# Performance work log

Measured on AMD Instinct MI355X. Metric: run time of the kernel, lower is better.

Reference implementation:

```python
import jax, jax.numpy as jnp
import numpy as np

B, T, C, N = 4, 2048, 1024, 16
D = C // N


def setup_inputs() -> dict:
    key = jax.random.key(0)
    ks = jax.random.split(key, 10)
    s = 1.0 / np.sqrt(C)
    x = jax.random.normal(ks[0], (B, T, C), dtype=jnp.float32)
    token_mask = jax.random.randint(ks[1], (B, T), 0, 2, dtype=jnp.int32)
    token_mask = token_mask.at[:, 0].set(1)  # keep col 0 valid so no all--inf row
    inp = {"x": x, "token_mask": token_mask}
    for i, name in enumerate(["q", "k", "v", "p"]):
        inp[f"w{name}"] = jax.random.uniform(ks[2 + 2 * i], (C, C), jnp.float32, -s, s)
        inp[f"b{name}"] = jax.random.uniform(ks[3 + 2 * i], (C,), jnp.float32, -s, s)
    return inp


def reference(x, token_mask, wq, bq, wk, bk, wv, bv, wp, bp):
    # projections: nn.Linear computes x @ W.T + b
    q = (x @ wq.T + bq).reshape(B, T, N, D)
    k = (x @ wk.T + bk).reshape(B, T, N, D)
    v = (x @ wv.T + bv).reshape(B, T, N, D)
    # scores: (B, N, T, T)
    scores = jnp.einsum("bqnd,bknd->bnqk", q, k) / jnp.sqrt(jnp.float32(D))
    causal = jnp.tril(jnp.ones((T, T), dtype=bool))
    valid = causal[None, None] & (token_mask[:, None, None, :] != 0)
    scores = jnp.where(valid, scores, -jnp.inf)
    probs = jax.nn.softmax(scores, axis=-1)
    attn = jnp.einsum("bnqk,bknd->bqnd", probs, v).reshape(B, T, C)
    out = attn @ wp.T + bp
    return out
```

## Files before the change

kernel.cpp:

```cpp
#include <hip/hip_runtime.h>
#include <math.h>

typedef short bf16x8 __attribute__((ext_vector_type(8)));
typedef float f32x4 __attribute__((ext_vector_type(4)));

__device__ __forceinline__ unsigned short f2bf(float f) {
    union { float f; unsigned u; } v; v.f = f;
    unsigned r = v.u + 0x7fffu + ((v.u >> 16) & 1u);
    return (unsigned short)(r >> 16);
}

__device__ __forceinline__ void gld_lds16(const unsigned short* g, const unsigned short* l) {
    __builtin_amdgcn_global_load_lds(
        (const __attribute__((address_space(1))) void*)g,
        (__attribute__((address_space(3))) void*)l, 16, 0, 0);
}

__global__ void cvt_f32_bf16(const float* __restrict__ src, unsigned short* __restrict__ dst, int n) {
    int i = (blockIdx.x * blockDim.x + threadIdx.x) * 4;
    if (i < n) {
        float4 f = *(const float4*)(src + i);
        ushort4 o;
        o.x = f2bf(f.x); o.y = f2bf(f.y); o.z = f2bf(f.z); o.w = f2bf(f.w);
        *(ushort4*)(dst + i) = o;
    }
}

__global__ void cvt4_f32_bf16(const float* s0, const float* s1, const float* s2, const float* s3,
                              unsigned short* d0, unsigned short* d1, unsigned short* d2,
                              unsigned short* d3, int n) {
    const float* s; unsigned short* d;
    switch (blockIdx.y) {
        case 0: s = s0; d = d0; break;
        case 1: s = s1; d = d1; break;
        case 2: s = s2; d = d2; break;
        default: s = s3; d = d3; break;
    }
    int i = (blockIdx.x * blockDim.x + threadIdx.x) * 4;
    if (i < n) {
        float4 f = *(const float4*)(s + i);
        ushort4 o;
        o.x = f2bf(f.x); o.y = f2bf(f.y); o.z = f2bf(f.z); o.w = f2bf(f.w);
        *(ushort4*)(d + i) = o;
    }
}

__global__ __launch_bounds__(256) void gemm_bt(
        const unsigned short* __restrict__ A, const unsigned short* __restrict__ W,
        const float* __restrict__ bias, float* __restrict__ outF,
        unsigned short* __restrict__ outB, int M, int N, int K) {
    __shared__ __align__(16) unsigned short As[128][32];
    __shared__ __align__(16) unsigned short Ws[128][32];
    const int m0 = blockIdx.y * 128, n0 = blockIdx.x * 128;
    const int tid = threadIdx.x, lane = tid & 63, w = tid >> 6;
    const int quad = lane >> 4, lc = lane & 15;
    const int wr = (w >> 1) * 64, wc = (w & 1) * 64;
    const int sr = lane >> 2, sc = (lane & 3) * 8;

    f32x4 acc[4][4] = {};

    for (int k0 = 0; k0 < K; k0 += 32) {
        __syncthreads();
        gld_lds16(A + (size_t)(m0 + w * 32 +      sr) * K + k0 + sc, &As[w * 32     ][0]);
        gld_lds16(A + (size_t)(m0 + w * 32 + 16 + sr) * K + k0 + sc, &As[w * 32 + 16][0]);
        gld_lds16(W + (size_t)(n0 + w * 32 +      sr) * K + k0 + sc, &Ws[w * 32     ][0]);
        gld_lds16(W + (size_t)(n0 + w * 32 + 16 + sr) * K + k0 + sc, &Ws[w * 32 + 16][0]);
        __syncthreads();
        bf16x8 af[4], bw[4];
        #pragma unroll
        for (int i = 0; i < 4; ++i) af[i] = *(const bf16x8*)&As[wr + i * 16 + lc][quad * 8];
        #pragma unroll
        for (int j = 0; j < 4; ++j) bw[j] = *(const bf16x8*)&Ws[wc + j * 16 + lc][quad * 8];
        #pragma unroll
        for (int i = 0; i < 4; ++i)
            #pragma unroll
            for (int j = 0; j < 4; ++j)
                acc[i][j] = __builtin_amdgcn_mfma_f32_16x16x32_bf16(af[i], bw[j], acc[i][j], 0, 0, 0);
    }

    #pragma unroll
    for (int j = 0; j < 4; ++j) {
        int col = n0 + wc + j * 16 + lc;
        float bj = bias[col];
        #pragma unroll
        for (int i = 0; i < 4; ++i) {
            int rowb = m0 + wr + i * 16 + quad * 4;
            #pragma unroll
            for (int r = 0; r < 4; ++r) {
                float v = acc[i][j][r] + bj;
                size_t idx = (size_t)(rowb + r) * N + col;
                if (outB) outB[idx] = f2bf(v);
                else      outF[idx] = v;
            }
        }
    }
}

__global__ __launch_bounds__(256, 4) void attn_kernel(
        const unsigned short* __restrict__ Q, const unsigned short* __restrict__ K,
        const unsigned short* __restrict__ V, const int* __restrict__ tmask,
        unsigned short* __restrict__ O) {
    const int T = 2048, C = 1024;
    __shared__ __align__(16) unsigned short Kl[64][72];
    __shared__ __align__(16) unsigned short VT[64][72];
    __shared__ __align__(16) unsigned short Pl[4][16][72];
    __shared__ float maskf[64];

    const int pair = blockIdx.x;
    const int bn = blockIdx.y;
    const int b = bn >> 4, h = bn & 15;
    const int tid = threadIdx.x, w = tid >> 6, lane = tid & 63;
    const int quad = lane >> 4, lc = lane & 15;
    const float NEG_INF = -__builtin_inff();

    #pragma unroll 1
    for (int half = 0; half < 2; ++half) {
        const int qt = half ? (31 - pair) : pair;

        size_t qrow = (size_t)(b * T + qt * 64 + w * 16 + lc) * C + h * 64;
        bf16x8 qb0 = *(const bf16x8*)(Q + qrow + quad * 8);
        bf16x8 qb1 = *(const bf16x8*)(Q + qrow + 32 + quad * 8);

        f32x4 oaccT[4] = {};
        float m = NEG_INF, l = 0.f;
        const int qg = qt * 64 + w * 16 + lc;

        for (int kt = 0; kt <= qt; ++kt) {
            __syncthreads();
            {
                int r = tid >> 2, c16 = (tid & 3) * 16;
                size_t g = (size_t)(b * T + kt * 64 + r) * C + h * 64 + c16;
                *(bf16x8*)&Kl[r][c16]     = *(const bf16x8*)(K + g);
                *(bf16x8*)&Kl[r][c16 + 8] = *(const bf16x8*)(K + g + 8);
            }
            {
                int r0 = (tid & 31) * 2, c8 = (tid >> 5) * 8;
                size_t g = (size_t)(b * T + kt * 64 + r0) * C + h * 64 + c8;
                bf16x8 v0 = *(const bf16x8*)(V + g);
                bf16x8 v1 = *(const bf16x8*)(V + g + C);
                #pragma unroll
                for (int i = 0; i < 8; ++i) {
                    unsigned pk = (unsigned short)v0[i] | ((unsigned)(unsigned short)v1[i] << 16);
                    *(unsigned*)&VT[c8 + i][r0] = pk;
                }
            }
            if (tid < 64)
                maskf[tid] = tmask[b * T + kt * 64 + tid] ? 0.0f : NEG_INF;
            __syncthreads();

            f32x4 sacc[4] = {};
            #pragma unroll
            for (int j = 0; j < 4; ++j) {
                bf16x8 ka0 = *(const bf16x8*)&Kl[j * 16 + lc][quad * 8];
                bf16x8 ka1 = *(const bf16x8*)&Kl[j * 16 + lc][32 + quad * 8];
                sacc[j] = __builtin_amdgcn_mfma_f32_16x16x32_bf16(ka0, qb0, sacc[j], 0, 0, 0);
                sacc[j] = __builtin_amdgcn_mfma_f32_16x16x32_bf16(ka1, qb1, sacc[j], 0, 0, 0);
            }

            float s[4][4];
            float mx = NEG_INF;
            #pragma unroll
            for (int j = 0; j < 4; ++j) {
                f32x4 mk = *(const f32x4*)&maskf[j * 16 + quad * 4];
                #pragma unroll
                for (int r = 0; r < 4; ++r) {
                    int kg = kt * 64 + j * 16 + quad * 4 + r;
                    float sv = sacc[j][r] * 0.125f + mk[r];
                    if (kg > qg) sv = NEG_INF;
                    s[j][r] = sv;
                    mx = fmaxf(mx, sv);
                }
            }
            mx = fmaxf(mx, __shfl_xor(mx, 16, 64));
            mx = fmaxf(mx, __shfl_xor(mx, 32, 64));
            float mnew = fmaxf(m, mx);
            float alpha = __expf(m - mnew);
            m = mnew;
            float ps = 0.f;
            #pragma unroll
            for (int j = 0; j < 4; ++j)
                #pragma unroll
                for (int r = 0; r < 4; ++r) {
                    float p = __expf(s[j][r] - mnew);
                    s[j][r] = p;
                    ps += p;
                }
            ps += __shfl_xor(ps, 16, 64);
            ps += __shfl_xor(ps, 32, 64);
            l = l * alpha + ps;
            #pragma unroll
            for (int jd = 0; jd < 4; ++jd) oaccT[jd] *= alpha;

            #pragma unroll
            for (int j = 0; j < 4; ++j) {
                ushort4 pk;
                pk.x = f2bf(s[j][0]); pk.y = f2bf(s[j][1]);
                pk.z = f2bf(s[j][2]); pk.w = f2bf(s[j][3]);
                *(ushort4*)&Pl[w][lc][j * 16 + quad * 4] = pk;
            }
            bf16x8 pb0 = *(const bf16x8*)&Pl[w][lc][quad * 8];
            bf16x8 pb1 = *(const bf16x8*)&Pl[w][lc][32 + quad * 8];

            #pragma unroll
            for (int jd = 0; jd < 4; ++jd) {
                bf16x8 va0 = *(const bf16x8*)&VT[jd * 16 + lc][quad * 8];
                bf16x8 va1 = *(const bf16x8*)&VT[jd * 16 + lc][32 + quad * 8];
                oaccT[jd] = __builtin_amdgcn_mfma_f32_16x16x32_bf16(va0, pb0, oaccT[jd], 0, 0, 0);
                oaccT[jd] = __builtin_amdgcn_mfma_f32_16x16x32_bf16(va1, pb1, oaccT[jd], 0, 0, 0);
            }
        }

        float inv = 1.0f / l;
        size_t orow = (size_t)(b * T + qt * 64 + w * 16 + lc) * C + h * 64;
        #pragma unroll
        for (int jd = 0; jd < 4; ++jd) {
            ushort4 o4;
            o4.x = f2bf(oaccT[jd][0] * inv);
            o4.y = f2bf(oaccT[jd][1] * inv);
            o4.z = f2bf(oaccT[jd][2] * inv);
            o4.w = f2bf(oaccT[jd][3] * inv);
            *(ushort4*)(O + orow + jd * 16 + quad * 4) = o4;
        }
    }
}

extern "C" void kernel_launch(void* const* d_in, const int* in_sizes, int n_in,
                              void* d_out, int out_size, void* d_ws, size_t ws_size,
                              hipStream_t stream) {
    const float* x  = (const float*)d_in[0];
    const int* tm   = (const int*)d_in[1];
    const float* wq = (const float*)d_in[2]; const float* bq = (const float*)d_in[3];
    const float* wk = (const float*)d_in[4]; const float* bk = (const float*)d_in[5];
    const float* wv = (const float*)d_in[6]; const float* bv = (const float*)d_in[7];
    const float* wp = (const float*)d_in[8]; const float* bp = (const float*)d_in[9];
    float* out = (float*)d_out;

    const int Bv = 4, Tv = 2048, Cv = 1024;
    const size_t MT = (size_t)Bv * Tv;
    const size_t XN = MT * Cv;
    const size_t WN = (size_t)Cv * Cv;

    unsigned short* xb  = (unsigned short*)d_ws;
    unsigned short* wqb = xb  + XN;
    unsigned short* wkb = wqb + WN;
    unsigned short* wvb = wkb + WN;
    unsigned short* wpb = wvb + WN;
    unsigned short* Qb  = wpb + WN;
    unsigned short* Kb  = Qb + XN;
    unsigned short* Vb  = Kb + XN;
    unsigned short* Ab  = xb;

    cvt_f32_bf16<<<XN / 1024, 256, 0, stream>>>(x, xb, (int)XN);
    cvt4_f32_bf16<<<dim3(WN / 1024, 4), 256, 0, stream>>>(wq, wk, wv, wp, wqb, wkb, wvb, wpb, (int)WN);

    dim3 gg(Cv / 128, MT / 128);
    gemm_bt<<<gg, 256, 0, stream>>>(xb, wqb, bq, nullptr, Qb, (int)MT, Cv, Cv);
    gemm_bt<<<gg, 256, 0, stream>>>(xb, wkb, bk, nullptr, Kb, (int)MT, Cv, Cv);
    gemm_bt<<<gg, 256, 0, stream>>>(xb, wvb, bv, nullptr, Vb, (int)MT, Cv, Cv);

    attn_kernel<<<dim3(16, Bv * 16), 256, 0, stream>>>(Qb, Kb, Vb, tm, Ab);

    gemm_bt<<<gg, 256, 0, stream>>>(Ab, wpb, bp, out, nullptr, (int)MT, Cv, Cv);
}
```

Measured before the change: 336.3 us.

## Fuse QKV projections into one GEMM launch and restructure attention grid

Merges the three Q/K/V projection GEMMs into one launch over a 3072-wide output, relying on the Q/K/V weight buffers being contiguous and routing each column block to its bias and output buffer. The attention kernel now gives each block one query tile instead of a balanced pair, launches twice as many blocks with a higher occupancy hint, and hoists the causal mask check so it runs only on the diagonal tile. The scale is folded into an exp2-based softmax, and probabilities are packed with a paired bf16 conversion. The one-tile-per-block split drops the pairwise load balancing, so block run times now vary with the query tile.

```diff
diff --git a/kernel.cpp b/kernel.cpp
--- a/kernel.cpp
+++ b/kernel.cpp
@@ -1,13 +1,26 @@
 #include <hip/hip_runtime.h>
+#include <hip/hip_bf16.h>
 #include <math.h>
 
 typedef short bf16x8 __attribute__((ext_vector_type(8)));
 typedef float f32x4 __attribute__((ext_vector_type(4)));
+
+#if __has_builtin(__builtin_amdgcn_exp2f)
+#define EXP2F(x) __builtin_amdgcn_exp2f(x)
+#else
+#define EXP2F(x) __expf(0.69314718056f * (x))
+#endif
 
 __device__ __forceinline__ unsigned short f2bf(float f) {
     union { float f; unsigned u; } v; v.f = f;
     unsigned r = v.u + 0x7fffu + ((v.u >> 16) & 1u);
     return (unsigned short)(r >> 16);
+}
+
+__device__ __forceinline__ unsigned pack_bf2(float a, float b) {
+    __hip_bfloat162 h = __float22bfloat162_rn(float2{a, b});
+    union { __hip_bfloat162 h; unsigned u; } c; c.h = h;
+    return c.u;
 }
 
 __device__ __forceinline__ void gld_lds16(const unsigned short* g, const unsigned short* l) {
@@ -47,16 +60,21 @@
 
 __global__ __launch_bounds__(256) void gemm_bt(
         const unsigned short* __restrict__ A, const unsigned short* __restrict__ W,
-        const float* __restrict__ bias, float* __restrict__ outF,
-        unsigned short* __restrict__ outB, int M, int N, int K) {
+        const float* __restrict__ b0p, const float* __restrict__ b1p,
+        const float* __restrict__ b2p, float* __restrict__ outF,
+        unsigned short* __restrict__ outB, int M, int Nlog, int K) {
     __shared__ __align__(16) unsigned short As[128][32];
     __shared__ __align__(16) unsigned short Ws[128][32];
+    const size_t BUFS = (size_t)8192 * 1024;
     const int m0 = blockIdx.y * 128, n0 = blockIdx.x * 128;
     const int tid = threadIdx.x, lane = tid & 63, w = tid >> 6;
     const int quad = lane >> 4, lc = lane & 15;
     const int wr = (w >> 1) * 64, wc = (w & 1) * 64;
     const int sr = lane >> 2, sc = (lane & 3) * 8;
 
+    const int buf = n0 >> 10;
+    const float* bias = buf == 0 ? b0p : (buf == 1 ? b1p : b2p);
+
     f32x4 acc[4][4] = {};
 
     for (int k0 = 0; k0 < K; k0 += 32) {
@@ -81,14 +99,15 @@
     #pragma unroll
     for (int j = 0; j < 4; ++j) {
         int col = n0 + wc + j * 16 + lc;
-        float bj = bias[col];
+        int coll = col & 1023;
+        float bj = bias[coll];
         #pragma unroll
         for (int i = 0; i < 4; ++i) {
             int rowb = m0 + wr + i * 16 + quad * 4;
             #pragma unroll
             for (int r = 0; r < 4; ++r) {
                 float v = acc[i][j][r] + bj;
-                size_t idx = (size_t)(rowb + r) * N + col;
+                size_t idx = (size_t)buf * BUFS + (size_t)(rowb + r) * 1024 + coll;
                 if (outB) outB[idx] = f2bf(v);
                 else      outF[idx] = v;
             }
@@ -96,7 +115,7 @@
     }
 }
 
-__global__ __launch_bounds__(256, 4) void attn_kernel(
+__global__ __launch_bounds__(256, 5) void attn_kernel(
         const unsigned short* __restrict__ Q, const unsigned short* __restrict__ K,
         const unsigned short* __restrict__ V, const int* __restrict__ tmask,
         unsigned short* __restrict__ O) {
@@ -106,121 +125,123 @@
     __shared__ __align__(16) unsigned short Pl[4][16][72];
     __shared__ float maskf[64];
 
-    const int pair = blockIdx.x;
+    const int qt = 31 - blockIdx.x;
     const int bn = blockIdx.y;
     const int b = bn >> 4, h = bn & 15;
     const int tid = threadIdx.x, w = tid >> 6, lane = tid & 63;
     const int quad = lane >> 4, lc = lane & 15;
     const float NEG_INF = -__builtin_inff();
+    const float CSC = 0.18033688011112042f;
+
+    size_t qrow = (size_t)(b * T + qt * 64 + w * 16 + lc) * C + h * 64;
+    bf16x8 qb0 = *(const bf16x8*)(Q + qrow + quad * 8);
+    bf16x8 qb1 = *(const bf16x8*)(Q + qrow + 32 + quad * 8);
+
+    f32x4 oaccT[4] = {};
+    float m = NEG_INF, l = 0.f;
+    const int qg = qt * 64 + w * 16 + lc;
+
+    auto step = [&](int kt, bool DIAG) {
+        __syncthreads();
+        {
+            int r = tid >> 2, c16 = (tid & 3) * 16;
+            size_t g = (size_t)(b * T + kt * 64 + r) * C + h * 64 + c16;
+            *(bf16x8*)&Kl[r][c16]     = *(const bf16x8*)(K + g);
+            *(bf16x8*)&Kl[r][c16 + 8] = *(const bf16x8*)(K + g + 8);
+        }
+        {
+            int r0 = (tid & 31) * 2, c8 = (tid >> 5) * 8;
+            size_t g = (size_t)(b * T + kt * 64 + r0) * C + h * 64 + c8;
+            bf16x8 v0 = *(const bf16x8*)(V + g);
+            bf16x8 v1 = *(const bf16x8*)(V + g + C);
+            #pragma unroll
+            for (int i = 0; i < 8; ++i) {
+                unsigned pk = (unsigned short)v0[i] | ((unsigned)(unsigned short)v1[i] << 16);
+                *(unsigned*)&VT[c8 + i][r0] = pk;
+            }
+        }
+        if (tid < 64)
+            maskf[tid] = tmask[b * T + kt * 64 + tid] ? 0.0f : NEG_INF;
+        __syncthreads();
+
+        f32x4 sacc[4] = {};
+        #pragma unroll
+        for (int j = 0; j < 4; ++j) {
+            bf16x8 ka0 = *(const bf16x8*)&Kl[j * 16 + lc][quad * 8];
+            bf16x8 ka1 = *(const bf16x8*)&Kl[j * 16 + lc][32 + quad * 8];
+            sacc[j] = __builtin_amdgcn_mfma_f32_16x16x32_bf16(ka0, qb0, sacc[j], 0, 0, 0);
+            sacc[j] = __builtin_amdgcn_mfma_f32_16x16x32_bf16(ka1, qb1, sacc[j], 0, 0, 0);
+        }
+
+        float s[4][4];
+        float mx = NEG_INF;
+        #pragma unroll
+        for (int j = 0; j < 4; ++j) {
+            f32x4 mk = *(const f32x4*)&maskf[j * 16 + quad * 4];
+            #pragma unroll
+            for (int r = 0; r < 4; ++r) {
+                float sv = fmaf(sacc[j][r], CSC, mk[r]);
+                if (DIAG) {
+                    int kg = kt * 64 + j * 16 + quad * 4 + r;
+                    if (kg > qg) sv = NEG_INF;
+                }
+                s[j][r] = sv;
+                mx = fmaxf(mx, sv);
+            }
+        }
+        mx = fmaxf(mx, __shfl_xor(mx, 16, 64));
+        mx = fmaxf(mx, __shfl_xor(mx, 32, 64));
+        float mnew = fmaxf(m, mx);
+        float alpha = EXP2F(m - mnew);
+        m = mnew;
+        float ps = 0.f;
+        #pragma unroll
+        for (int j = 0; j < 4; ++j)
+            #pragma unroll
+            for (int r = 0; r < 4; ++r) {
+                float p = EXP2F(s[j][r] - mnew);
+                s[j][r] = p;
+                ps += p;
+            }
+        ps += __shfl_xor(ps, 16, 64);
+        ps += __shfl_xor(ps, 32, 64);
+        l = l * alpha + ps;
+        #pragma unroll
+        for (int jd = 0; jd < 4; ++jd) oaccT[jd] *= alpha;
+
+        #pragma unroll
+        for (int j = 0; j < 4; ++j) {
+            uint2 pk;
+            pk.x = pack_bf2(s[j][0], s[j][1]);
+            pk.y = pack_bf2(s[j][2], s[j][3]);
+            *(uint2*)&Pl[w][lc][j * 16 + quad * 4] = pk;
+        }
+        bf16x8 pb0 = *(const bf16x8*)&Pl[w][lc][quad * 8];
+        bf16x8 pb1 = *(const bf16x8*)&Pl[w][lc][32 + quad * 8];
+
+        #pragma unroll
+        for (int jd = 0; jd < 4; ++jd) {
+            bf16x8 va0 = *(const bf16x8*)&VT[jd * 16 + lc][quad * 8];
+            bf16x8 va1 = *(const bf16x8*)&VT[jd * 16 + lc][32 + quad * 8];
+            oaccT[jd] = __builtin_amdgcn_mfma_f32_16x16x32_bf16(va0, pb0, oaccT[jd], 0, 0, 0);
+            oaccT[jd] = __builtin_amdgcn_mfma_f32_16x16x32_bf16(va1, pb1, oaccT[jd], 0, 0, 0);
+        }
+    };
 
     #pragma unroll 1
-    for (int half = 0; half < 2; ++half) {
-        const int qt = half ? (31 - pair) : pair;
-
-        size_t qrow = (size_t)(b * T + qt * 64 + w * 16 + lc) * C + h * 64;
-        bf16x8 qb0 = *(const bf16x8*)(Q + qrow + quad * 8);
-        bf16x8 qb1 = *(const bf16x8*)(Q + qrow + 32 + quad * 8);
-
-        f32x4 oaccT[4] = {};
-        float m = NEG_INF, l = 0.f;
-        const int qg = qt * 64 + w * 16 + lc;
-
-        for (int kt = 0; kt <= qt; ++kt) {
-            __syncthreads();
-            {
-                int r = tid >> 2, c16 = (tid & 3) * 16;
-                size_t g = (size_t)(b * T + kt * 64 + r) * C + h * 64 + c16;
-                *(bf16x8*)&Kl[r][c16]     = *(const bf16x8*)(K + g);
-                *(bf16x8*)&Kl[r][c16 + 8] = *(const bf16x8*)(K + g + 8);
-            }
-            {
-                int r0 = (tid & 31) * 2, c8 = (tid >> 5) * 8;
-                size_t g = (size_t)(b * T + kt * 64 + r0) * C + h * 64 + c8;
-                bf16x8 v0 = *(const bf16x8*)(V + g);
-                bf16x8 v1 = *(const bf16x8*)(V + g + C);
-                #pragma unroll
-                for (int i = 0; i < 8; ++i) {
-                    unsigned pk = (unsigned short)v0[i] | ((unsigned)(unsigned short)v1[i] << 16);
-                    *(unsigned*)&VT[c8 + i][r0] = pk;
-                }
-            }
-            if (tid < 64)
-                maskf[tid] = tmask[b * T + kt * 64 + tid] ? 0.0f : NEG_INF;
-            __syncthreads();
-
-            f32x4 sacc[4] = {};
-            #pragma unroll
-            for (int j = 0; j < 4; ++j) {
-                bf16x8 ka0 = *(const bf16x8*)&Kl[j * 16 + lc][quad * 8];
-                bf16x8 ka1 = *(const bf16x8*)&Kl[j * 16 + lc][32 + quad * 8];
-                sacc[j] = __builtin_amdgcn_mfma_f32_16x16x32_bf16(ka0, qb0, sacc[j], 0, 0, 0);
-                sacc[j] = __builtin_amdgcn_mfma_f32_16x16x32_bf16(ka1, qb1, sacc[j], 0, 0, 0);
-            }
-
-            float s[4][4];
-            float mx = NEG_INF;
-            #pragma unroll
-            for (int j = 0; j < 4; ++j) {
-                f32x4 mk = *(const f32x4*)&maskf[j * 16 + quad * 4];
-                #pragma unroll
-                for (int r = 0; r < 4; ++r) {
-                    int kg = kt * 64 + j * 16 + quad * 4 + r;
-                    float sv = sacc[j][r] * 0.125f + mk[r];
-                    if (kg > qg) sv = NEG_INF;
-                    s[j][r] = sv;
-                    mx = fmaxf(mx, sv);
-                }
-            }
-            mx = fmaxf(mx, __shfl_xor(mx, 16, 64));
-            mx = fmaxf(mx, __shfl_xor(mx, 32, 64));
-            float mnew = fmaxf(m, mx);
-            float alpha = __expf(m - mnew);
-            m = mnew;
-            float ps = 0.f;
-            #pragma unroll
-            for (int j = 0; j < 4; ++j)
-                #pragma unroll
-                for (int r = 0; r < 4; ++r) {
-                    float p = __expf(s[j][r] - mnew);
-                    s[j][r] = p;
-                    ps += p;
-                }
-            ps += __shfl_xor(ps, 16, 64);
-            ps += __shfl_xor(ps, 32, 64);
-            l = l * alpha + ps;
-            #pragma unroll
-            for (int jd = 0; jd < 4; ++jd) oaccT[jd] *= alpha;
-
-            #pragma unroll
-            for (int j = 0; j < 4; ++j) {
-                ushort4 pk;
-                pk.x = f2bf(s[j][0]); pk.y = f2bf(s[j][1]);
-                pk.z = f2bf(s[j][2]); pk.w = f2bf(s[j][3]);
-                *(ushort4*)&Pl[w][lc][j * 16 + quad * 4] = pk;
-            }
-            bf16x8 pb0 = *(const bf16x8*)&Pl[w][lc][quad * 8];
-            bf16x8 pb1 = *(const bf16x8*)&Pl[w][lc][32 + quad * 8];
-
-            #pragma unroll
-            for (int jd = 0; jd < 4; ++jd) {
-                bf16x8 va0 = *(const bf16x8*)&VT[jd * 16 + lc][quad * 8];
-                bf16x8 va1 = *(const bf16x8*)&VT[jd * 16 + lc][32 + quad * 8];
-                oaccT[jd] = __builtin_amdgcn_mfma_f32_16x16x32_bf16(va0, pb0, oaccT[jd], 0, 0, 0);
-                oaccT[jd] = __builtin_amdgcn_mfma_f32_16x16x32_bf16(va1, pb1, oaccT[jd], 0, 0, 0);
-            }
-        }
-
-        float inv = 1.0f / l;
-        size_t orow = (size_t)(b * T + qt * 64 + w * 16 + lc) * C + h * 64;
-        #pragma unroll
-        for (int jd = 0; jd < 4; ++jd) {
-            ushort4 o4;
-            o4.x = f2bf(oaccT[jd][0] * inv);
-            o4.y = f2bf(oaccT[jd][1] * inv);
-            o4.z = f2bf(oaccT[jd][2] * inv);
-            o4.w = f2bf(oaccT[jd][3] * inv);
-            *(ushort4*)(O + orow + jd * 16 + quad * 4) = o4;
-        }
+    for (int kt = 0; kt < qt; ++kt) step(kt, false);
+    step(qt, true);
+
+    float inv = 1.0f / l;
+    size_t orow = (size_t)(b * T + qt * 64 + w * 16 + lc) * C + h * 64;
+    #pragma unroll
+    for (int jd = 0; jd < 4; ++jd) {
+        ushort4 o4;
+        o4.x = f2bf(oaccT[jd][0] * inv);
+        o4.y = f2bf(oaccT[jd][1] * inv);
+        o4.z = f2bf(oaccT[jd][2] * inv);
+        o4.w = f2bf(oaccT[jd][3] * inv);
+        *(ushort4*)(O + orow + jd * 16 + quad * 4) = o4;
     }
 }
 
@@ -253,12 +274,9 @@
     cvt_f32_bf16<<<XN / 1024, 256, 0, stream>>>(x, xb, (int)XN);
     cvt4_f32_bf16<<<dim3(WN / 1024, 4), 256, 0, stream>>>(wq, wk, wv, wp, wqb, wkb, wvb, wpb, (int)WN);
 
-    dim3 gg(Cv / 128, MT / 128);
-    gemm_bt<<<gg, 256, 0, stream>>>(xb, wqb, bq, nullptr, Qb, (int)MT, Cv, Cv);
-    gemm_bt<<<gg, 256, 0, stream>>>(xb, wkb, bk, nullptr, Kb, (int)MT, Cv, Cv);
-    gemm_bt<<<gg, 256, 0, stream>>>(xb, wvb, bv, nullptr, Vb, (int)MT, Cv, Cv);
-
-    attn_kernel<<<dim3(16, Bv * 16), 256, 0, stream>>>(Qb, Kb, Vb, tm, Ab);
-
-    gemm_bt<<<gg, 256, 0, stream>>>(Ab, wpb, bp, out, nullptr, (int)MT, Cv, Cv);
-}
+    gemm_bt<<<dim3(24, 64), 256, 0, stream>>>(xb, wqb, bq, bk, bv, nullptr, Qb, (int)MT, 3072, Cv);
+
+    attn_kernel<<<dim3(32, Bv * 16), 256, 0, stream>>>(Qb, Kb, Vb, tm, Ab);
+
+    gemm_bt<<<dim3(8, 64), 256, 0, stream>>>(Ab, wpb, bp, bp, bp, out, nullptr, (int)MT, 1024, Cv);
+}
```

Result: slower. 363.1 us (+8.0%).
